# Kernel optimization log

Measured on AMD Instinct MI355X. Metric: run time of the kernel, lower is better.

The kernel has to match this reference:

```python
import jax, jax.numpy as jnp
import numpy as np

B = 4096          # batch
N_REPS = 16       # number of irreducible reps (all same d here)
N_ELEMS = 128     # group elements per rep
D = 32            # block dimension
N_SYMBOLS = 64    # alphabet size
EMB = N_REPS * D * D  # 16384


def setup_inputs() -> dict:
    key = jax.random.key(0)
    k1, k2, k3, k4 = jax.random.split(key, 4)
    state_embedding = jax.random.normal(k1, (B, EMB), dtype=jnp.float32)
    input_symbols = jax.random.randint(k2, (B,), 0, N_SYMBOLS, dtype=jnp.int64)
    reps = jax.random.normal(k3, (N_REPS, N_ELEMS, D, D), dtype=jnp.float32)
    transitions = jax.random.randint(k4, (N_SYMBOLS,), 0, N_ELEMS, dtype=jnp.int64)
    return {"state_embedding": state_embedding, "input_symbols": input_symbols,
            "reps": reps, "transitions": transitions}


def reference(state_embedding, input_symbols, reps, transitions):
    # state_embedding: [B, n_reps*d*d]; reps: [n_reps, n_elems, d, d]
    n_reps, n_elems, d, _ = reps.shape
    b = state_embedding.shape[0]
    # Split embedding into block-diagonal d x d blocks (all reps same d).
    blocks = jnp.nan_to_num(state_embedding.reshape(b, n_reps, d, d))  # [b, r, d, d]
    # Per-symbol gather: symbol -> group element -> rep matrix.
    t = transitions[input_symbols]            # [b]
    M = jnp.nan_to_num(reps[:, t])            # [r, b, d, d]
    # Per-matrix Frobenius normalization (matches rep_matrix.norm()).
    fro = jnp.sqrt(jnp.sum(M * M, axis=(-2, -1), keepdims=True))
    M = M / (fro + 1e-6)
    # Block-diagonal batched matmul: block @ rep_matrix per (batch, rep).
    out = jnp.einsum('brij,rbjk->brik', blocks, M)  # [b, r, d, d]
    return out.reshape(b, -1)
```

## Files before the change

### kernel.cpp

```cpp
#include <hip/hip_runtime.h>
#include <hip/hip_bf16.h>

#define NREPS   16
#define NELEMS  128
#define DD      32
#define MATSZ   (DD * DD)
#define EMB     (NREPS * MATSZ)

typedef __attribute__((ext_vector_type(8))) short bf16x8;
typedef __attribute__((ext_vector_type(4))) float f32x4;

static __device__ __forceinline__ short f2bf(float f) {
    __hip_bfloat16 h = __float2bfloat16(f);
    return *reinterpret_cast<short*>(&h);
}

__global__ __launch_bounds__(256) void prep_kernel(
    const float* __restrict__ reps, ushort* __restrict__ Mt)
{
    __shared__ float lM[DD * 33];
    __shared__ float red[4];
    const int mat = blockIdx.x;
    const int t   = threadIdx.x;

    float4 v = reinterpret_cast<const float4*>(reps + (size_t)mat * MATSZ)[t];
    const int i  = t >> 3;
    const int c0 = (t & 7) << 2;
    lM[i * 33 + c0 + 0] = v.x;
    lM[i * 33 + c0 + 1] = v.y;
    lM[i * 33 + c0 + 2] = v.z;
    lM[i * 33 + c0 + 3] = v.w;

    float s = v.x * v.x + v.y * v.y + v.z * v.z + v.w * v.w;
    #pragma unroll
    for (int off = 32; off; off >>= 1) s += __shfl_xor(s, off, 64);
    if ((t & 63) == 0) red[t >> 6] = s;
    __syncthreads();
    const float scale = 1.0f / (sqrtf(red[0] + red[1] + red[2] + red[3]) + 1e-6f);

    const int col = t >> 3;
    const int k0  = (t & 7) << 2;
    ushort4 o;
    o.x = (ushort)f2bf(lM[(k0 + 0) * 33 + col] * scale);
    o.y = (ushort)f2bf(lM[(k0 + 1) * 33 + col] * scale);
    o.z = (ushort)f2bf(lM[(k0 + 2) * 33 + col] * scale);
    o.w = (ushort)f2bf(lM[(k0 + 3) * 33 + col] * scale);
    reinterpret_cast<ushort4*>(Mt + (size_t)mat * MATSZ)[t] = o;
}

__global__ __launch_bounds__(256) void trans_mfma_kernel(
    const float*  __restrict__ emb,
    const int*    __restrict__ syms,
    const ushort* __restrict__ Mt,
    const int*    __restrict__ trans,
    float*        __restrict__ out)
{
    const int bid = blockIdx.x;
    const int b   = bid >> 2;
    const int w   = threadIdx.x >> 6;
    const int l   = threadIdx.x & 63;
    const int r   = ((bid & 3) << 2) | w;

    const int esym = trans[syms[b]];
    const int lr = l & 15;
    const int k0 = (l >> 4) << 3;

    const float*  A  = emb + (size_t)b * EMB + (size_t)r * MATSZ;
    const ushort* Mw = Mt + ((size_t)r * NELEMS + esym) * MATSZ;

    bf16x8 af[2];
    #pragma unroll
    for (int ti = 0; ti < 2; ++ti) {
        const float* ap = A + (ti * 16 + lr) * DD + k0;
        float4 lo = *reinterpret_cast<const float4*>(ap);
        float4 hi = *reinterpret_cast<const float4*>(ap + 4);
        bf16x8 f;
        f[0] = f2bf(lo.x); f[1] = f2bf(lo.y); f[2] = f2bf(lo.z); f[3] = f2bf(lo.w);
        f[4] = f2bf(hi.x); f[5] = f2bf(hi.y); f[6] = f2bf(hi.z); f[7] = f2bf(hi.w);
        af[ti] = f;
    }

    bf16x8 bfg[2];
    #pragma unroll
    for (int tj = 0; tj < 2; ++tj)
        bfg[tj] = *reinterpret_cast<const bf16x8*>(Mw + (tj * 16 + lr) * DD + k0);

    const f32x4 z = {0.0f, 0.0f, 0.0f, 0.0f};
    f32x4 acc[2][2];
    #pragma unroll
    for (int ti = 0; ti < 2; ++ti)
        #pragma unroll
        for (int tj = 0; tj < 2; ++tj)
            acc[ti][tj] = __builtin_amdgcn_mfma_f32_16x16x32_bf16(
                af[ti], bfg[tj], z, 0, 0, 0);

    float* Ob = out + (size_t)b * EMB + (size_t)r * MATSZ;
    const int row0 = (l >> 4) << 2;
    #pragma unroll
    for (int ti = 0; ti < 2; ++ti)
        #pragma unroll
        for (int m = 0; m < 4; ++m) {
            const int row = ti * 16 + row0 + m;
            #pragma unroll
            for (int tj = 0; tj < 2; ++tj)
                Ob[row * DD + tj * 16 + lr] = acc[ti][tj][m];
        }
}

extern "C" void kernel_launch(void* const* d_in, const int* in_sizes, int n_in,
                              void* d_out, int out_size, void* d_ws, size_t ws_size,
                              hipStream_t stream) {
    const float* emb   = (const float*)d_in[0];
    const int*   syms  = (const int*)d_in[1];
    const float* reps  = (const float*)d_in[2];
    const int*   trans = (const int*)d_in[3];
    float*  outp = (float*)d_out;
    ushort* Mt   = (ushort*)d_ws;

    const int B = in_sizes[1];

    hipLaunchKernelGGL(prep_kernel, dim3(NREPS * NELEMS), dim3(256), 0, stream,
                       reps, Mt);
    hipLaunchKernelGGL(trans_mfma_kernel, dim3(B * 4), dim3(256), 0, stream,
                       emb, syms, Mt, trans, outp);
}
```

Baseline: 107.3 us.

## Fuse rep normalization and transpose into main MFMA kernel, drop prep pass

Removes the separate prep kernel that normalized and transposed every rep matrix into a bf16 workspace. Each wave now reads its fp32 rep matrix directly with strided column loads, computes the Frobenius norm with a wave reduction, and applies the scale to the MFMA output. Output stores become nontemporal. This saves one launch and a full pass over all 2048 rep matrices, at the cost of uncoalesced strided loads and redundant norm computation per batch row.

```diff
diff --git a/kernel.cpp b/kernel.cpp
--- a/kernel.cpp
+++ b/kernel.cpp
@@ -15,45 +15,12 @@
     return *reinterpret_cast<short*>(&h);
 }
 
-__global__ __launch_bounds__(256) void prep_kernel(
-    const float* __restrict__ reps, ushort* __restrict__ Mt)
-{
-    __shared__ float lM[DD * 33];
-    __shared__ float red[4];
-    const int mat = blockIdx.x;
-    const int t   = threadIdx.x;
-
-    float4 v = reinterpret_cast<const float4*>(reps + (size_t)mat * MATSZ)[t];
-    const int i  = t >> 3;
-    const int c0 = (t & 7) << 2;
-    lM[i * 33 + c0 + 0] = v.x;
-    lM[i * 33 + c0 + 1] = v.y;
-    lM[i * 33 + c0 + 2] = v.z;
-    lM[i * 33 + c0 + 3] = v.w;
-
-    float s = v.x * v.x + v.y * v.y + v.z * v.z + v.w * v.w;
-    #pragma unroll
-    for (int off = 32; off; off >>= 1) s += __shfl_xor(s, off, 64);
-    if ((t & 63) == 0) red[t >> 6] = s;
-    __syncthreads();
-    const float scale = 1.0f / (sqrtf(red[0] + red[1] + red[2] + red[3]) + 1e-6f);
-
-    const int col = t >> 3;
-    const int k0  = (t & 7) << 2;
-    ushort4 o;
-    o.x = (ushort)f2bf(lM[(k0 + 0) * 33 + col] * scale);
-    o.y = (ushort)f2bf(lM[(k0 + 1) * 33 + col] * scale);
-    o.z = (ushort)f2bf(lM[(k0 + 2) * 33 + col] * scale);
-    o.w = (ushort)f2bf(lM[(k0 + 3) * 33 + col] * scale);
-    reinterpret_cast<ushort4*>(Mt + (size_t)mat * MATSZ)[t] = o;
-}
-
-__global__ __launch_bounds__(256) void trans_mfma_kernel(
-    const float*  __restrict__ emb,
-    const int*    __restrict__ syms,
-    const ushort* __restrict__ Mt,
-    const int*    __restrict__ trans,
-    float*        __restrict__ out)
+__global__ __launch_bounds__(256) void trans_fused_mfma_kernel(
+    const float* __restrict__ emb,
+    const int*   __restrict__ syms,
+    const float* __restrict__ reps,
+    const int*   __restrict__ trans,
+    float*       __restrict__ out)
 {
     const int bid = blockIdx.x;
     const int b   = bid >> 2;
@@ -65,8 +32,8 @@
     const int lr = l & 15;
     const int k0 = (l >> 4) << 3;
 
-    const float*  A  = emb + (size_t)b * EMB + (size_t)r * MATSZ;
-    const ushort* Mw = Mt + ((size_t)r * NELEMS + esym) * MATSZ;
+    const float* A = emb  + (size_t)b * EMB + (size_t)r * MATSZ;
+    const float* M = reps + ((size_t)r * NELEMS + esym) * MATSZ;
 
     bf16x8 af[2];
     #pragma unroll
@@ -80,10 +47,23 @@
         af[ti] = f;
     }
 
+    float ss = 0.0f;
     bf16x8 bfg[2];
     #pragma unroll
-    for (int tj = 0; tj < 2; ++tj)
-        bfg[tj] = *reinterpret_cast<const bf16x8*>(Mw + (tj * 16 + lr) * DD + k0);
+    for (int tj = 0; tj < 2; ++tj) {
+        const float* mp = M + tj * 16 + lr;
+        float mv[8];
+        #pragma unroll
+        for (int kk = 0; kk < 8; ++kk)
+            mv[kk] = mp[(k0 + kk) * DD];
+        bf16x8 f;
+        #pragma unroll
+        for (int kk = 0; kk < 8; ++kk) {
+            ss += mv[kk] * mv[kk];
+            f[kk] = f2bf(mv[kk]);
+        }
+        bfg[tj] = f;
+    }
 
     const f32x4 z = {0.0f, 0.0f, 0.0f, 0.0f};
     f32x4 acc[2][2];
@@ -94,6 +74,14 @@
             acc[ti][tj] = __builtin_amdgcn_mfma_f32_16x16x32_bf16(
                 af[ti], bfg[tj], z, 0, 0, 0);
 
+    ss += __shfl_xor(ss, 1, 64);
+    ss += __shfl_xor(ss, 2, 64);
+    ss += __shfl_xor(ss, 4, 64);
+    ss += __shfl_xor(ss, 8, 64);
+    ss += __shfl_xor(ss, 16, 64);
+    ss += __shfl_xor(ss, 32, 64);
+    const float scale = 1.0f / (sqrtf(ss) + 1e-6f);
+
     float* Ob = out + (size_t)b * EMB + (size_t)r * MATSZ;
     const int row0 = (l >> 4) << 2;
     #pragma unroll
@@ -103,7 +91,8 @@
             const int row = ti * 16 + row0 + m;
             #pragma unroll
             for (int tj = 0; tj < 2; ++tj)
-                Ob[row * DD + tj * 16 + lr] = acc[ti][tj][m];
+                __builtin_nontemporal_store(acc[ti][tj][m] * scale,
+                                            Ob + row * DD + tj * 16 + lr);
         }
 }
 
@@ -114,13 +103,10 @@
     const int*   syms  = (const int*)d_in[1];
     const float* reps  = (const float*)d_in[2];
     const int*   trans = (const int*)d_in[3];
-    float*  outp = (float*)d_out;
-    ushort* Mt   = (ushort*)d_ws;
+    float* outp = (float*)d_out;
 
     const int B = in_sizes[1];
 
-    hipLaunchKernelGGL(prep_kernel, dim3(NREPS * NELEMS), dim3(256), 0, stream,
-                       reps, Mt);
-    hipLaunchKernelGGL(trans_mfma_kernel, dim3(B * 4), dim3(256), 0, stream,
-                       emb, syms, Mt, trans, outp);
+    hipLaunchKernelGGL(trans_fused_mfma_kernel, dim3(B * 4), dim3(256), 0, stream,
+                       emb, syms, reps, trans, outp);
 }
```

After: 114.8 us. +6.9%, slower.
